# Performance work log

Measured on AMD Instinct MI355X. Metric: run time of the kernel, lower is better.

## Reference

```python
import jax, jax.numpy as jnp
import numpy as np

T, X_D, M_N, CHUNK, REDUCE = 2048, 2048, 64, 64, 8
M_D = X_D // REDUCE          # 256
DECAY_D = M_D // 4           # 64
H_D = X_D * 2                # factor=2
FF_D = 256 * round(int(H_D * (2.0 / 3.0)) / 256)  # 2816


def setup_inputs() -> dict:
    key = jax.random.key(0)
    ks = jax.random.split(key, 20)
    def lin(k, out_d, in_d):
        return (jax.random.normal(k, (out_d, in_d), jnp.float32) / np.sqrt(in_d).astype(np.float32))
    return {
        "xs": jax.random.normal(ks[0], (T, X_D), jnp.float32),
        "attn_q": lin(ks[1], X_D // REDUCE, X_D),
        "attn_k": lin(ks[2], X_D // REDUCE, X_D // REDUCE),
        "attn_v": lin(ks[3], X_D, X_D),
        "attn_o": lin(ks[4], X_D, X_D),
        "attn_r": lin(ks[5], X_D, X_D),
        "mem_f": lin(ks[6], M_N, X_D),
        "mem_q": lin(ks[7], M_D, X_D),
        "mem_k": lin(ks[8], M_D, M_D),
        "mem_v": lin(ks[9], M_D, X_D),
        "mem_o": lin(ks[10], X_D, M_D),
        "mem_r": lin(ks[11], X_D, X_D),
        "mem_beta": -jnp.ones((M_N, M_D), jnp.float32),
        "mem_decay": 3.0 * jnp.ones((M_N, DECAY_D), jnp.float32),
        "mem_l": jax.random.uniform(ks[12], (M_N, M_D), dtype=jnp.float32),
        "ff_in1": lin(ks[13], FF_D, X_D),
        "ff_in2": lin(ks[14], FF_D, X_D),
        "ff_out": lin(ks[15], X_D, FF_D),
        "sn1_g": jnp.sqrt(jnp.float32(X_D)),
        "sn2_g": jnp.sqrt(jnp.float32(X_D)),
    }


def _rotate_half(x):
    x1 = x[..., ::2]
    x2 = x[..., 1::2]
    return jnp.stack((-x2, x1), axis=-1).reshape(x.shape)


def _scale_norm(x, g):
    return x * (g / (jnp.linalg.norm(x, axis=-1, keepdims=True) + 1e-8))


def _attn(xs, Wq, Wk, Wv, Wo, Wr):
    n = CHUNK
    q = xs @ Wq.T                       # (T, dk)
    k = q @ Wk.T                        # k is computed from q (as in source)
    v = xs @ Wv.T                       # (T, x_d)
    c = xs.shape[0] // n
    dk = q.shape[-1]
    q = q.reshape(c, n, dk)
    k = k.reshape(c, n, dk)
    v = v.reshape(c, n, v.shape[-1])

    def with_prev(a):                   # prepend previous chunk (zero for chunk 0)
        prev = jnp.concatenate([jnp.zeros_like(a[:1]), a[:-1]], axis=0)
        return jnp.concatenate([prev, a], axis=1)   # (c, 2n, d)

    k2, v2 = with_prev(k), with_prev(v)

    # RoPE over 2n key positions; queries take the last n positions
    inv_freq = 1.0 / (10000.0 ** (jnp.arange(0, dk, 2, dtype=jnp.float32) / dk))
    ang = jnp.arange(2 * n, dtype=jnp.float32)[:, None] * inv_freq[None, :]
    sin = jnp.repeat(jnp.sin(ang), 2, axis=-1)      # (2n, dk) interleaved
    cos = jnp.repeat(jnp.cos(ang), 2, axis=-1)
    q = q * cos[None, n:] + _rotate_half(q) * sin[None, n:]
    k2 = k2 * cos[None] + _rotate_half(k2) * sin[None]

    qk = jnp.einsum('cnk,cmk->cnm', q, k2) / jnp.sqrt(jnp.float32(dk))
    allowed = jnp.arange(2 * n)[None, :] <= (jnp.arange(n)[:, None] + n)  # tril offset n
    A = jax.nn.softmax(jnp.where(allowed[None], qk, -jnp.inf), axis=-1)
    y = jnp.einsum('cnm,cmv->cnv', A, v2).reshape(xs.shape[0], -1)
    return (y @ Wo.T) * jax.nn.sigmoid(xs @ Wr.T)


def _mem(xs, Wf, Wq, Wk, Wv, Wo, Wr, beta_p, decay_p, l_p):
    v = xs @ Wv.T                                       # (T, m_d)
    f = jax.nn.sigmoid(xs @ Wf.T)[:, :, None]           # (T, m_n, 1)
    beta = jax.nn.sigmoid(beta_p)[None]                 # (1, m_n, m_d)
    gamma = jnp.concatenate(
        [jnp.ones((M_N, M_D - DECAY_D), xs.dtype), jax.nn.sigmoid(decay_p)], axis=1
    )[None]                                             # (1, m_n, m_d)
    ws = (1.0 - f * beta) * gamma                       # (T, m_n, m_d)
    fvs = f * v[:, None, :]                             # (T, m_n, m_d)

    def bin_assoc(ei, ej):
        ai, bi = ei
        aj, bj = ej
        return (aj * ai, aj * bi + bj)

    _, mems = jax.lax.associative_scan(bin_assoc, (ws, fvs), axis=0)  # (T, m_n, m_d)

    q = xs @ Wq.T                                       # (T, m_d)
    k = jnp.einsum('nmd,kd->nmk', mems, Wk) + l_p[None]
    A = jax.nn.softmax(jnp.einsum('nmk,nk->nm', k, q) / jnp.sqrt(jnp.float32(M_D)), axis=-1)
    y = jnp.einsum('nm,nmd->nd', A, mems)
    return (y @ Wo.T) * jax.nn.sigmoid(xs @ Wr.T)


def _ff(xs, W1, W2, Wo):
    return (jax.nn.silu(xs @ W1.T) * (xs @ W2.T)) @ Wo.T


def reference(xs, attn_q, attn_k, attn_v, attn_o, attn_r,
              mem_f, mem_q, mem_k, mem_v, mem_o, mem_r,
              mem_beta, mem_decay, mem_l,
              ff_in1, ff_in2, ff_out, sn1_g, sn2_g):
    xn = _scale_norm(xs, sn1_g)
    xs = (_attn(xn, attn_q, attn_k, attn_v, attn_o, attn_r)
          + _mem(xn, mem_f, mem_q, mem_k, mem_v, mem_o, mem_r, mem_beta, mem_decay, mem_l)
          + xs)
    xs = _ff(_scale_norm(xs, sn2_g), ff_in1, ff_in2, ff_out) + xs
    return xs
```

## Files before the change

kernel.cpp:

```cpp
#include <hip/hip_runtime.h>
#include <math.h>


typedef short bhalf8 __attribute__((ext_vector_type(8)));
typedef float f32x4 __attribute__((ext_vector_type(4)));

#define CC_LD 7168
#define COL_V   0
#define COL_B1  2048
#define COL_B2  4096
#define COL_QB  6144
#define COL_VM  6400
#define COL_QM  6656
#define COL_FG  6912

#define AS1 __attribute__((address_space(1)))
#define AS3 __attribute__((address_space(3)))

__device__ __forceinline__ float sigmoidf_(float x){ return 1.0f/(1.0f+expf(-x)); }

__device__ __forceinline__ unsigned short f2b(float f){
  unsigned u = __float_as_uint(f);
  unsigned r = (u + 0x7fffu + ((u>>16)&1u)) >> 16;
  return (unsigned short)r;
}
__device__ __forceinline__ float b2f(unsigned short h){
  return __uint_as_float(((unsigned)h)<<16);
}

__global__ __launch_bounds__(256) void k_prep(
    const float* __restrict__ av, const float* __restrict__ ar, const float* __restrict__ mr,
    const float* __restrict__ aq, const float* __restrict__ mv, const float* __restrict__ mq,
    const float* __restrict__ mf, const float* __restrict__ ao, const float* __restrict__ mo,
    const float* __restrict__ f1, const float* __restrict__ f2, const float* __restrict__ fo,
    const float* __restrict__ ak, const float* __restrict__ mk,
    const float* __restrict__ xsrc, const float* __restrict__ g1,
    unsigned short* __restrict__ WCAT, unsigned short* __restrict__ AOB,
    unsigned short* __restrict__ MOB, unsigned short* __restrict__ FFW,
    unsigned short* __restrict__ FFOB, unsigned short* __restrict__ AKB,
    unsigned short* __restrict__ MKTB, float2* __restrict__ TR,
    unsigned short* __restrict__ XNb){
  int bid = blockIdx.x, tid = threadIdx.x;
  if (bid < 35520){
    int i = bid*256 + tid;
    const float* s; unsigned short* d; int off;
    if (i < 3571712){
      d = WCAT + (size_t)i*4;
      if      (i < 1048576){ s = av; off = i; }
      else if (i < 2097152){ s = ar; off = i-1048576; }
      else if (i < 3145728){ s = mr; off = i-2097152; }
      else if (i < 3276800){ s = aq; off = i-3145728; }
      else if (i < 3407872){ s = mv; off = i-3276800; }
      else if (i < 3538944){ s = mq; off = i-3407872; }
      else                 { s = mf; off = i-3538944; }
    }
    else if (i < 4620288){ off = i-3571712; s = ao; d = AOB  + (size_t)off*4; }
    else if (i < 4751360){ off = i-4620288; s = mo; d = MOB  + (size_t)off*4; }
    else if (i < 6193152){ off = i-4751360; s = f1;
      int row = off >> 9, c4 = off & 511;
      d = FFW + ((size_t)row*2)*2048 + c4*4; }
    else if (i < 7634944){ off = i-6193152; s = f2;
      int row = off >> 9, c4 = off & 511;
      d = FFW + ((size_t)row*2 + 1)*2048 + c4*4; }
    else if (i < 9076736){ off = i-7634944; s = fo; d = FFOB + (size_t)off*4; }
    else if (i < 9093120){ off = i-9076736; s = ak; d = AKB  + (size_t)off*4; }
    else return;
    float4 v = ((const float4*)s)[off];
    ushort4 o;
    o.x = f2b(v.x); o.y = f2b(v.y); o.z = f2b(v.z); o.w = f2b(v.w);
    *(ushort4*)d = o;
  } else if (bid < 35776){
    int i = bid - 35520, j = tid;
    MKTB[(size_t)j*256 + i] = f2b(mk[(size_t)i*256 + j]);
  } else if (bid < 35840){
    int idx = (bid - 35776)*256 + tid;
    int pos = idx >> 7, j = idx & 127;
    float inv = powf(10000.f, -(float)j/128.f);
    float a = (float)pos * inv;
    TR[idx] = make_float2(cosf(a), sinf(a));
  } else {
    int row = bid - 35840;
    const float* xr = xsrc + (size_t)row*2048;
    float ss = 0.f;
    for (int j = tid; j < 2048; j += 256){ float v = xr[j]; ss += v*v; }
    __shared__ float red[256];
    red[tid] = ss; __syncthreads();
    for (int s = 128; s > 0; s >>= 1){ if (tid < s) red[tid] += red[tid+s]; __syncthreads(); }
    float scale = g1[0] / (sqrtf(red[0]) + 1e-8f);
    unsigned short* orow = XNb + (size_t)row*2048;
    for (int j4 = tid; j4 < 512; j4 += 256){
      float4 v = *(const float4*)(xr + j4*4);
      ushort4 o;
      o.x = f2b(v.x*scale); o.y = f2b(v.y*scale); o.z = f2b(v.z*scale); o.w = f2b(v.w*scale);
      ((ushort4*)orow)[j4] = o;
    }
  }
}

__global__ __launch_bounds__(256) void k_scalenorm_b(const float* __restrict__ x,
    const float* __restrict__ g, unsigned short* __restrict__ ob){
  int row = blockIdx.x, tid = threadIdx.x;
  const float* xr = x + (size_t)row*2048;
  float ss = 0.f;
  for (int j = tid; j < 2048; j += 256){ float v = xr[j]; ss += v*v; }
  __shared__ float red[256];
  red[tid] = ss; __syncthreads();
  for (int s = 128; s > 0; s >>= 1){ if (tid < s) red[tid] += red[tid+s]; __syncthreads(); }
  float scale = g[0] / (sqrtf(red[0]) + 1e-8f);
  unsigned short* orow = ob + (size_t)row*2048;
  for (int j4 = tid; j4 < 512; j4 += 256){
    float4 v = *(const float4*)(xr + j4*4);
    ushort4 o;
    o.x = f2b(v.x*scale); o.y = f2b(v.y*scale); o.z = f2b(v.z*scale); o.w = f2b(v.w*scale);
    ((ushort4*)orow)[j4] = o;
  }
}

__global__ __launch_bounds__(256) void k_gemm_p(
    const unsigned short* __restrict__ A, int lda,
    const unsigned short* __restrict__ B,
    float* __restrict__ C, unsigned short* __restrict__ Cb,
    int N, int K, int ldc, int epi,
    const float* __restrict__ add,
    const unsigned short* __restrict__ gate, int gate_ld,
    const unsigned short* A2, const unsigned short* B2, float* C2){
  __shared__ unsigned short LDSu[24576];
  int tid = threadIdx.x;
  int w = tid >> 6, l = tid & 63;
  int bi = blockIdx.y, bj = blockIdx.x;
  const unsigned short* Ap = A; const unsigned short* Bp = B; float* Cp = C;
  if (blockIdx.z){ Ap = A2; Bp = B2; Cp = C2; }
  int m0 = bi*128, n0 = bj*128;
  int wr = w >> 1, wc = w & 1;

  f32x4 acc[4][4];
#pragma unroll
  for (int i=0;i<4;++i)
#pragma unroll
    for (int j=0;j<4;++j){ f32x4 z = {0.f,0.f,0.f,0.f}; acc[i][j] = z; }

  const int r0 = tid >> 2;
  const int gsrc8 = (((tid&3) ^ ((tid>>3)&3)) * 8);

  auto stage = [&](int bs, int kt){
    unsigned short* db = LDSu + bs*8192;
    const unsigned short* ap0 = Ap + (size_t)(m0 + r0)*lda      + kt*32 + gsrc8;
    const unsigned short* ap1 = Ap + (size_t)(m0 + 64 + r0)*lda + kt*32 + gsrc8;
    const unsigned short* bp0 = Bp + (size_t)(n0 + r0)*K        + kt*32 + gsrc8;
    const unsigned short* bp1 = Bp + (size_t)(n0 + 64 + r0)*K   + kt*32 + gsrc8;
    __builtin_amdgcn_global_load_lds((const AS1 void*)ap0, (AS3 void*)(db + tid*8),        16, 0, 0);
    __builtin_amdgcn_global_load_lds((const AS1 void*)ap1, (AS3 void*)(db + 2048 + tid*8), 16, 0, 0);
    __builtin_amdgcn_global_load_lds((const AS1 void*)bp0, (AS3 void*)(db + 4096 + tid*8), 16, 0, 0);
    __builtin_amdgcn_global_load_lds((const AS1 void*)bp1, (AS3 void*)(db + 6144 + tid*8), 16, 0, 0);
  };

  const int nt = K >> 5;
  stage(0, 0);
  stage(1, 1);
  asm volatile("s_waitcnt vmcnt(4)" ::: "memory");
  __builtin_amdgcn_s_barrier();

  const int lr = l & 15;
  const int gsw = (((l>>4) ^ ((l>>1)&3)) * 8);
  const int aoff = (wr*64 + lr)*32 + gsw;
  const int boff = 4096 + (wc*64 + lr)*32 + gsw;

  int cur = 0;
  for (int t = 0; t < nt; ++t){
    if (t + 2 < nt) stage((t+2)%3, t+2);
    const unsigned short* Tb = LDSu + cur*8192;
    bhalf8 af[4], bfr[4];
#pragma unroll
    for (int m=0;m<4;++m) af[m]  = *(const bhalf8*)(Tb + aoff + m*512);
#pragma unroll
    for (int n=0;n<4;++n) bfr[n] = *(const bhalf8*)(Tb + boff + n*512);
    __builtin_amdgcn_s_setprio(1);
#pragma unroll
    for (int m=0;m<4;++m)
#pragma unroll
      for (int n=0;n<4;++n)
        acc[m][n] = __builtin_amdgcn_mfma_f32_16x16x32_bf16(af[m], bfr[n], acc[m][n], 0, 0, 0);
    __builtin_amdgcn_s_setprio(0);
    if (t + 1 < nt){
      if (t + 2 < nt){ asm volatile("s_waitcnt vmcnt(4)" ::: "memory"); }
      else           { asm volatile("s_waitcnt vmcnt(0)" ::: "memory"); }
      __builtin_amdgcn_s_barrier();
      cur = (cur == 2) ? 0 : cur + 1;
    }
  }

#pragma unroll
  for (int m=0;m<4;++m){
    int rowb = m0 + wr*64 + m*16 + ((l>>4)<<2);
#pragma unroll
    for (int r=0;r<4;++r){
      int row = rowb + r;
      size_t rbase = (size_t)row*ldc;
      size_t gbase = (size_t)row*gate_ld;
#pragma unroll
      for (int n=0;n<4;++n){
        int col = n0 + wc*64 + n*16 + (l&15);
        float v = acc[m][n][r];
        if (add) v += add[rbase + col];
        if (epi == 2) v *= sigmoidf_(b2f(gate[gbase + col]));
        if (epi == 3) Cb[rbase + col] = f2b(v);
        else          Cp[rbase + col] = v;
      }
    }
  }
}

__global__ __launch_bounds__(256) void k_combo1(
    const unsigned short* __restrict__ CCb_, const unsigned short* __restrict__ AKB,
    const unsigned short* __restrict__ MKTB, float* __restrict__ K0f, float* __restrict__ QHf,
    const float* __restrict__ beta_p, const float* __restrict__ decay_p,
    float* __restrict__ CP, float* __restrict__ CQ){
  int bid = blockIdx.x, tid = threadIdx.x;
  if (bid < 64){
    __shared__ unsigned short LDSu[24576];
    int w = tid >> 6, l = tid & 63;
    int zz = bid >> 5, bi = (bid >> 1) & 15, bj = bid & 1;
    const unsigned short* Ap = zz ? (CCb_ + COL_QM) : (CCb_ + COL_QB);
    const unsigned short* Bp = zz ? MKTB : AKB;
    float* Cp = zz ? QHf : K0f;
    const int lda = CC_LD, K = 256, ldc = 256;
    int m0 = bi*128, n0 = bj*128;
    int wr = w >> 1, wc = w & 1;

    f32x4 acc[4][4];
#pragma unroll
    for (int i=0;i<4;++i)
#pragma unroll
      for (int j=0;j<4;++j){ f32x4 z = {0.f,0.f,0.f,0.f}; acc[i][j] = z; }

    const int r0 = tid >> 2;
    const int gsrc8 = (((tid&3) ^ ((tid>>3)&3)) * 8);

    auto stage = [&](int bs, int kt){
      unsigned short* db = LDSu + bs*8192;
      const unsigned short* ap0 = Ap + (size_t)(m0 + r0)*lda      + kt*32 + gsrc8;
      const unsigned short* ap1 = Ap + (size_t)(m0 + 64 + r0)*lda + kt*32 + gsrc8;
      const unsigned short* bp0 = Bp + (size_t)(n0 + r0)*K        + kt*32 + gsrc8;
      const unsigned short* bp1 = Bp + (size_t)(n0 + 64 + r0)*K   + kt*32 + gsrc8;
      __builtin_amdgcn_global_load_lds((const AS1 void*)ap0, (AS3 void*)(db + tid*8),        16, 0, 0);
      __builtin_amdgcn_global_load_lds((const AS1 void*)ap1, (AS3 void*)(db + 2048 + tid*8), 16, 0, 0);
      __builtin_amdgcn_global_load_lds((const AS1 void*)bp0, (AS3 void*)(db + 4096 + tid*8), 16, 0, 0);
      __builtin_amdgcn_global_load_lds((const AS1 void*)bp1, (AS3 void*)(db + 6144 + tid*8), 16, 0, 0);
    };

    const int nt = 8;
    stage(0, 0);
    stage(1, 1);
    asm volatile("s_waitcnt vmcnt(4)" ::: "memory");
    __builtin_amdgcn_s_barrier();

    const int lr = l & 15;
    const int gsw = (((l>>4) ^ ((l>>1)&3)) * 8);
    const int aoff = (wr*64 + lr)*32 + gsw;
    const int boff = 4096 + (wc*64 + lr)*32 + gsw;

    int cur = 0;
    for (int t = 0; t < nt; ++t){
      if (t + 2 < nt) stage((t+2)%3, t+2);
      const unsigned short* Tb = LDSu + cur*8192;
      bhalf8 af[4], bfr[4];
#pragma unroll
      for (int m=0;m<4;++m) af[m]  = *(const bhalf8*)(Tb + aoff + m*512);
#pragma unroll
      for (int n=0;n<4;++n) bfr[n] = *(const bhalf8*)(Tb + boff + n*512);
      __builtin_amdgcn_s_setprio(1);
#pragma unroll
      for (int m=0;m<4;++m)
#pragma unroll
        for (int n=0;n<4;++n)
          acc[m][n] = __builtin_amdgcn_mfma_f32_16x16x32_bf16(af[m], bfr[n], acc[m][n], 0, 0, 0);
      __builtin_amdgcn_s_setprio(0);
      if (t + 1 < nt){
        if (t + 2 < nt){ asm volatile("s_waitcnt vmcnt(4)" ::: "memory"); }
        else           { asm volatile("s_waitcnt vmcnt(0)" ::: "memory"); }
        __builtin_amdgcn_s_barrier();
        cur = (cur == 2) ? 0 : cur + 1;
      }
    }

#pragma unroll
    for (int m=0;m<4;++m){
      int rowb = m0 + wr*64 + m*16 + ((l>>4)<<2);
#pragma unroll
      for (int r=0;r<4;++r){
        size_t rbase = (size_t)(rowb + r)*ldc;
#pragma unroll
        for (int n=0;n<4;++n){
          int col = n0 + wc*64 + n*16 + (l&15);
          Cp[rbase + col] = acc[m][n][r];
        }
      }
    }
  } else {
    int idx = bid - 64;
    int c = idx >> 3, mg = idx & 7, d = tid;
    __shared__ float Fs[128];
    if (tid < 128){
      int s = tid >> 3, j = tid & 7;
      Fs[tid] = sigmoidf_(b2f(CCb_[(size_t)(c*16+s)*CC_LD + COL_FG + mg*8 + j]));
    }
    __syncthreads();
    float beta[8], gamma[8], Pa[8], Qa[8];
#pragma unroll
    for (int j=0;j<8;++j){
      int m = mg*8+j;
      beta[j]  = sigmoidf_(beta_p[m*256+d]);
      gamma[j] = (d < 192) ? 1.f : sigmoidf_(decay_p[m*64 + (d-192)]);
      Pa[j] = 1.f; Qa[j] = 0.f;
    }
    for (int s = 0; s < 16; ++s){
      float vm = b2f(CCb_[(size_t)(c*16+s)*CC_LD + COL_VM + d]);
#pragma unroll
      for (int j=0;j<8;++j){
        float f = Fs[s*8+j];
        float w = (1.f - f*beta[j])*gamma[j];
        Pa[j] *= w;
        Qa[j] = w*Qa[j] + f*vm;
      }
    }
#pragma unroll
    for (int j=0;j<8;++j){
      size_t oidx = ((size_t)c*64 + mg*8 + j)*256 + d;
      CP[oidx] = Pa[j]; CQ[oidx] = Qa[j];
    }
  }
}

__global__ __launch_bounds__(256) void k_combo2(
    const unsigned short* __restrict__ CCqb, const float* __restrict__ K0,
    const float2* __restrict__ TR, unsigned short* __restrict__ P,
    const float* __restrict__ CP, const float* __restrict__ CQ, float* __restrict__ SIN){
  int bid = blockIdx.x, tid = threadIdx.x;
  if (bid < 32){
    __shared__ unsigned short Ks[128*256];
    int c = bid;
    for (int it = 0; it < 16; ++it){
      int id = tid + it*256;
      int m = id >> 5;
      int cs = (id & 31) * 8;
      float v[8];
      if (c == 0 && m < 64){
#pragma unroll
        for (int u=0;u<8;++u) v[u] = 0.f;
      } else {
        int gr = (c-1)*64 + m;
        const float* kr = K0 + (size_t)gr*256 + cs;
        float4 x0 = *(const float4*)kr, x1 = *(const float4*)(kr+4);
        v[0]=x0.x; v[1]=x0.y; v[2]=x0.z; v[3]=x0.w;
        v[4]=x1.x; v[5]=x1.y; v[6]=x1.z; v[7]=x1.w;
#pragma unroll
        for (int p2=0;p2<4;++p2){
          float2 t = TR[m*128 + (cs>>1) + p2];
          float e = v[2*p2], o = v[2*p2+1];
          v[2*p2]   = e*t.x - o*t.y;
          v[2*p2+1] = o*t.x + e*t.y;
        }
      }
      unsigned short pk[8];
#pragma unroll
      for (int u=0;u<8;++u) pk[u] = f2b(v[u]);
      int byte = m*512 + ((cs*2) ^ ((m&7)<<4));
      *(bhalf8*)((char*)&Ks[0] + byte) = *(const bhalf8*)pk;
    }
    __syncthreads();

    int w = tid >> 6, l = tid & 63;
    int lr = l & 15, lkg = l >> 4;
    f32x4 acc[8];
#pragma unroll
    for (int n=0;n<8;++n){ f32x4 z = {0.f,0.f,0.f,0.f}; acc[n] = z; }

    int iq = w*16 + lr;
    const unsigned short* qbase = CCqb + (size_t)(c*64 + iq)*CC_LD;
    int pos = 64 + iq;

    for (int kt = 0; kt < 8; ++kt){
      int k0c = kt*32 + lkg*8;
      bhalf8 q8 = *(const bhalf8*)(qbase + k0c);
      float v[8];
#pragma unroll
      for (int u=0;u<8;++u) v[u] = b2f((unsigned short)(((short*)&q8)[u]));
#pragma unroll
      for (int p2=0;p2<4;++p2){
        float2 t = TR[pos*128 + (k0c>>1) + p2];
        float e = v[2*p2], o = v[2*p2+1];
        v[2*p2]   = e*t.x - o*t.y;
        v[2*p2+1] = o*t.x + e*t.y;
      }
      unsigned short pk[8];
#pragma unroll
      for (int u=0;u<8;++u) pk[u] = f2b(v[u]);
      bhalf8 af = *(const bhalf8*)pk;
#pragma unroll
      for (int n=0;n<8;++n){
        int m = n*16 + lr;
        int byte = m*512 + ((k0c*2) ^ ((m&7)<<4));
        bhalf8 bf = *(const bhalf8*)((const char*)&Ks[0] + byte);
        acc[n] = __builtin_amdgcn_mfma_f32_16x16x32_bf16(af, bf, acc[n], 0, 0, 0);
      }
    }

    int i0 = w*16 + lkg*4;
    float mx[4] = {-1e30f,-1e30f,-1e30f,-1e30f};
    float sm[4] = {0.f,0.f,0.f,0.f};
#pragma unroll
    for (int n=0;n<8;++n){
      int col = n*16 + lr;
#pragma unroll
      for (int r=0;r<4;++r){
        float vv = acc[n][r] * (1.f/16.f);
        if (col > i0 + r + 64) vv = -1e30f;
        acc[n][r] = vv;
        mx[r] = fmaxf(mx[r], vv);
      }
    }
#pragma unroll
    for (int s=1; s<16; s<<=1)
#pragma unroll
      for (int r=0;r<4;++r) mx[r] = fmaxf(mx[r], __shfl_xor(mx[r], s));
#pragma unroll
    for (int n=0;n<8;++n)
#pragma unroll
      for (int r=0;r<4;++r){
        float e = expf(acc[n][r] - mx[r]);
        acc[n][r] = e; sm[r] += e;
      }
#pragma unroll
    for (int s=1; s<16; s<<=1)
#pragma unroll
      for (int r=0;r<4;++r) sm[r] += __shfl_xor(sm[r], s);
    float rcp[4];
#pragma unroll
    for (int r=0;r<4;++r) rcp[r] = 1.f/sm[r];

    unsigned short* Pr = P + (size_t)c*8192;
#pragma unroll
    for (int n=0;n<8;++n){
      int col = n*16 + lr;
#pragma unroll
      for (int r=0;r<4;++r)
        Pr[(i0+r)*128 + col] = f2b(acc[n][r]*rcp[r]);
    }
  } else {
    int m = bid - 32, d = tid;
    float S = 0.f;
    for (int c = 0; c < 128; ++c){
      size_t idx = ((size_t)c*64 + m)*256 + d;
      SIN[idx] = S;
      S = CP[idx]*S + CQ[idx];
    }
  }
}

__global__ __launch_bounds__(256) void k_combo3(
    const unsigned short* __restrict__ P, const unsigned short* __restrict__ Vb, int vld,
    unsigned short* __restrict__ Y,
    const unsigned short* __restrict__ CC, const float* __restrict__ beta_p,
    const float* __restrict__ decay_p, const float* __restrict__ SIN,
    unsigned short* __restrict__ MEMS){
  int bid = blockIdx.x, tid = threadIdx.x;
  if (bid < 512){
    __shared__ unsigned short Vt[128*128];
    int ct = bid & 15, c = bid >> 4;
    {
      int k = tid >> 1;
      int ch = (tid & 1) * 64;
      if (c == 0 && k < 64){
        for (int u=0; u<64; ++u){
          int col = ch + u;
          int byte = col*256 + ((k*2) ^ ((col&7)<<4));
          *(unsigned short*)((char*)&Vt[0] + byte) = 0;
        }
      } else {
        int gr = (c-1)*64 + k;
        const unsigned short* vr = Vb + (size_t)gr*vld + ct*128 + ch;
        for (int u8=0; u8<8; ++u8){
          bhalf8 x = *(const bhalf8*)(vr + u8*8);
#pragma unroll
          for (int u=0;u<8;++u){
            int col = ch + u8*8 + u;
            int byte = col*256 + ((k*2) ^ ((col&7)<<4));
            *(unsigned short*)((char*)&Vt[0] + byte) = (unsigned short)(((short*)&x)[u]);
          }
        }
      }
    }
    __syncthreads();
    int w = tid >> 6, l = tid & 63, lr = l & 15, lkg = l >> 4;
    f32x4 acc[8];
#pragma unroll
    for (int n=0;n<8;++n){ f32x4 z = {0.f,0.f,0.f,0.f}; acc[n] = z; }
    const unsigned short* Pr = P + (size_t)c*8192;
    for (int kt=0; kt<4; ++kt){
      int kb = kt*32 + lkg*8;
      bhalf8 af = *(const bhalf8*)(Pr + (w*16 + lr)*128 + kb);
#pragma unroll
      for (int n=0;n<8;++n){
        int col = n*16 + lr;
        int byte = col*256 + ((kb*2) ^ ((col&7)<<4));
        bhalf8 bf = *(const bhalf8*)((const char*)&Vt[0] + byte);
        acc[n] = __builtin_amdgcn_mfma_f32_16x16x32_bf16(af, bf, acc[n], 0, 0, 0);
      }
    }
    int row0 = c*64 + w*16 + lkg*4;
#pragma unroll
    for (int n=0;n<8;++n){
      int col = ct*128 + n*16 + lr;
#pragma unroll
      for (int r=0;r<4;++r)
        Y[(size_t)(row0+r)*2048 + col] = f2b(acc[n][r]);
    }
  } else {
    int idx = bid - 512;
    int c = idx >> 3, mg = idx & 7, d = tid;
    __shared__ float Fs[128];
    if (tid < 128){
      int s = tid >> 3, j = tid & 7;
      Fs[tid] = sigmoidf_(b2f(CC[(size_t)(c*16+s)*CC_LD + COL_FG + mg*8 + j]));
    }
    __syncthreads();
    float beta[8], gamma[8], S[8];
#pragma unroll
    for (int j=0;j<8;++j){
      int m = mg*8+j;
      beta[j]  = sigmoidf_(beta_p[m*256+d]);
      gamma[j] = (d < 192) ? 1.f : sigmoidf_(decay_p[m*64 + (d-192)]);
      S[j] = SIN[((size_t)c*64 + m)*256 + d];
    }
    for (int s = 0; s < 16; ++s){
      float vm = b2f(CC[(size_t)(c*16+s)*CC_LD + COL_VM + d]);
      size_t tb = (size_t)(c*16+s)*64;
#pragma unroll
      for (int j=0;j<8;++j){
        float f = Fs[s*8+j];
        float w = (1.f - f*beta[j])*gamma[j];
        S[j] = w*S[j] + f*vm;
        MEMS[(tb + mg*8 + j)*256 + d] = f2b(S[j]);
      }
    }
  }
}

__global__ __launch_bounds__(256) void k_gemm_p64(
    const unsigned short* __restrict__ A, int lda,
    const unsigned short* __restrict__ B,
    float* __restrict__ C, int K, int ldc,
    const float* __restrict__ add){
  __shared__ unsigned short LDSu[18432];
  int tid = threadIdx.x;
  int w = tid >> 6, l = tid & 63;
  int bi = blockIdx.y, bj = blockIdx.x;
  int m0 = bi*128, n0 = bj*64;
  int wr = w >> 1, wc = w & 1;

  f32x4 acc[4][2];
#pragma unroll
  for (int i=0;i<4;++i)
#pragma unroll
    for (int j=0;j<2;++j){ f32x4 z = {0.f,0.f,0.f,0.f}; acc[i][j] = z; }

  const int r0 = tid >> 2;
  const int gsrc8 = (((tid&3) ^ ((tid>>3)&3)) * 8);

  auto stage = [&](int bs, int kt){
    unsigned short* db = LDSu + bs*6144;
    const unsigned short* ap0 = A + (size_t)(m0 + r0)*lda      + kt*32 + gsrc8;
    const unsigned short* ap1 = A + (size_t)(m0 + 64 + r0)*lda + kt*32 + gsrc8;
    const unsigned short* bp0 = B + (size_t)(n0 + r0)*K        + kt*32 + gsrc8;
    __builtin_amdgcn_global_load_lds((const AS1 void*)ap0, (AS3 void*)(db + tid*8),        16, 0, 0);
    __builtin_amdgcn_global_load_lds((const AS1 void*)ap1, (AS3 void*)(db + 2048 + tid*8), 16, 0, 0);
    __builtin_amdgcn_global_load_lds((const AS1 void*)bp0, (AS3 void*)(db + 4096 + tid*8), 16, 0, 0);
  };

  const int nt = K >> 5;
  stage(0, 0);
  stage(1, 1);
  asm volatile("s_waitcnt vmcnt(3)" ::: "memory");
  __builtin_amdgcn_s_barrier();

  const int lr = l & 15;
  const int gsw = (((l>>4) ^ ((l>>1)&3)) * 8);
  const int aoff = (wr*64 + lr)*32 + gsw;
  const int boff = 4096 + (wc*32 + lr)*32 + gsw;

  int cur = 0;
  for (int t = 0; t < nt; ++t){
    if (t + 2 < nt) stage((t+2)%3, t+2);
    const unsigned short* Tb = LDSu + cur*6144;
    bhalf8 af[4], bfr[2];
#pragma unroll
    for (int m=0;m<4;++m) af[m]  = *(const bhalf8*)(Tb + aoff + m*512);
#pragma unroll
    for (int n=0;n<2;++n) bfr[n] = *(const bhalf8*)(Tb + boff + n*512);
    __builtin_amdgcn_s_setprio(1);
#pragma unroll
    for (int m=0;m<4;++m)
#pragma unroll
      for (int n=0;n<2;++n)
        acc[m][n] = __builtin_amdgcn_mfma_f32_16x16x32_bf16(af[m], bfr[n], acc[m][n], 0, 0, 0);
    __builtin_amdgcn_s_setprio(0);
    if (t + 1 < nt){
      if (t + 2 < nt){ asm volatile("s_waitcnt vmcnt(3)" ::: "memory"); }
      else           { asm volatile("s_waitcnt vmcnt(0)" ::: "memory"); }
      __builtin_amdgcn_s_barrier();
      cur = (cur == 2) ? 0 : cur + 1;
    }
  }

#pragma unroll
  for (int m=0;m<4;++m){
    int rowb = m0 + wr*64 + m*16 + ((l>>4)<<2);
#pragma unroll
    for (int r=0;r<4;++r){
      int row = rowb + r;
      size_t rbase = (size_t)row*ldc;
#pragma unroll
      for (int n=0;n<2;++n){
        int col = n0 + wc*32 + n*16 + (l&15);
        C[rbase + col] = acc[m][n][r] + add[rbase + col];
      }
    }
  }
}

__global__ __launch_bounds__(256) void k_gemm_fuse2_64(
    const unsigned short* __restrict__ A,  const unsigned short* __restrict__ B,
    const unsigned short* __restrict__ A2, const unsigned short* __restrict__ B2,
    const unsigned short* __restrict__ gate1, const unsigned short* __restrict__ gate2,
    const float* __restrict__ xs, float* __restrict__ XS2){
  __shared__ unsigned short LDSu[18432];
  int tid = threadIdx.x;
  int w = tid >> 6, l = tid & 63;
  int bi = blockIdx.y, bj = blockIdx.x;
  int m0 = bi*128, n0 = bj*64;
  int wr = w >> 1, wc = w & 1;

  f32x4 acc[4][2], acc2[4][2];
#pragma unroll
  for (int i=0;i<4;++i)
#pragma unroll
    for (int j=0;j<2;++j){ f32x4 z = {0.f,0.f,0.f,0.f}; acc[i][j] = z; acc2[i][j] = z; }

  const int r0 = tid >> 2;
  const int gsrc8 = (((tid&3) ^ ((tid>>3)&3)) * 8);

  auto stage = [&](int bs, int kt, const unsigned short* Ap, int lda,
                   const unsigned short* Bp, int ldb){
    unsigned short* db = LDSu + bs*6144;
    const unsigned short* ap0 = Ap + (size_t)(m0 + r0)*lda      + kt*32 + gsrc8;
    const unsigned short* ap1 = Ap + (size_t)(m0 + 64 + r0)*lda + kt*32 + gsrc8;
    const unsigned short* bp0 = Bp + (size_t)(n0 + r0)*ldb      + kt*32 + gsrc8;
    __builtin_amdgcn_global_load_lds((const AS1 void*)ap0, (AS3 void*)(db + tid*8),        16, 0, 0);
    __builtin_amdgcn_global_load_lds((const AS1 void*)ap1, (AS3 void*)(db + 2048 + tid*8), 16, 0, 0);
    __builtin_amdgcn_global_load_lds((const AS1 void*)bp0, (AS3 void*)(db + 4096 + tid*8), 16, 0, 0);
  };

  const int lr = l & 15;
  const int gsw = (((l>>4) ^ ((l>>1)&3)) * 8);
  const int aoff = (wr*64 + lr)*32 + gsw;
  const int boff = 4096 + (wc*32 + lr)*32 + gsw;

  {
    const int nt = 64;
    stage(0, 0, A, 2048, B, 2048);
    stage(1, 1, A, 2048, B, 2048);
    asm volatile("s_waitcnt vmcnt(3)" ::: "memory");
    __builtin_amdgcn_s_barrier();
    int cur = 0;
    for (int t = 0; t < nt; ++t){
      if (t + 2 < nt) stage((t+2)%3, t+2, A, 2048, B, 2048);
      const unsigned short* Tb = LDSu + cur*6144;
      bhalf8 af[4], bfr[2];
#pragma unroll
      for (int m=0;m<4;++m) af[m]  = *(const bhalf8*)(Tb + aoff + m*512);
#pragma unroll
      for (int n=0;n<2;++n) bfr[n] = *(const bhalf8*)(Tb + boff + n*512);
      __builtin_amdgcn_s_setprio(1);
#pragma unroll
      for (int m=0;m<4;++m)
#pragma unroll
        for (int n=0;n<2;++n)
          acc[m][n] = __builtin_amdgcn_mfma_f32_16x16x32_bf16(af[m], bfr[n], acc[m][n], 0, 0, 0);
      __builtin_amdgcn_s_setprio(0);
      if (t + 1 < nt){
        if (t + 2 < nt){ asm volatile("s_waitcnt vmcnt(3)" ::: "memory"); }
        else           { asm volatile("s_waitcnt vmcnt(0)" ::: "memory"); }
        __builtin_amdgcn_s_barrier();
        cur = (cur == 2) ? 0 : cur + 1;
      }
    }
  }
  __syncthreads();

  {
    const int nt = 8;
    stage(0, 0, A2, 256, B2, 256);
    stage(1, 1, A2, 256, B2, 256);
    asm volatile("s_waitcnt vmcnt(3)" ::: "memory");
    __builtin_amdgcn_s_barrier();
    int cur = 0;
    for (int t = 0; t < nt; ++t){
      if (t + 2 < nt) stage((t+2)%3, t+2, A2, 256, B2, 256);
      const unsigned short* Tb = LDSu + cur*6144;
      bhalf8 af[4], bfr[2];
#pragma unroll
      for (int m=0;m<4;++m) af[m]  = *(const bhalf8*)(Tb + aoff + m*512);
#pragma unroll
      for (int n=0;n<2;++n) bfr[n] = *(const bhalf8*)(Tb + boff + n*512);
      __builtin_amdgcn_s_setprio(1);
#pragma unroll
      for (int m=0;m<4;++m)
#pragma unroll
        for (int n=0;n<2;++n)
          acc2[m][n] = __builtin_amdgcn_mfma_f32_16x16x32_bf16(af[m], bfr[n], acc2[m][n], 0, 0, 0);
      __builtin_amdgcn_s_setprio(0);
      if (t + 1 < nt){
        if (t + 2 < nt){ asm volatile("s_waitcnt vmcnt(3)" ::: "memory"); }
        else           { asm volatile("s_waitcnt vmcnt(0)" ::: "memory"); }
        __builtin_amdgcn_s_barrier();
        cur = (cur == 2) ? 0 : cur + 1;
      }
    }
  }

#pragma unroll
  for (int m=0;m<4;++m){
    int rowb = m0 + wr*64 + m*16 + ((l>>4)<<2);
#pragma unroll
    for (int r=0;r<4;++r){
      int row = rowb + r;
      size_t gb = (size_t)row*CC_LD;
      size_t rb = (size_t)row*2048;
#pragma unroll
      for (int n=0;n<2;++n){
        int col = n0 + wc*32 + n*16 + (l&15);
        float v = acc[m][n][r]*sigmoidf_(b2f(gate1[gb + col]))
                + acc2[m][n][r]*sigmoidf_(b2f(gate2[gb + col]))
                + xs[rb + col];
        XS2[rb + col] = v;
      }
    }
  }
}

__global__ __launch_bounds__(256) void k_gemm_silu(
    const unsigned short* __restrict__ A, int lda,
    const unsigned short* __restrict__ B,
    unsigned short* __restrict__ Cb, int K, int out_ld){
  __shared__ unsigned short LDSu[24576];
  int tid = threadIdx.x;
  int w = tid >> 6, l = tid & 63;
  int bi = blockIdx.y, bj = blockIdx.x;
  int m0 = bi*128, n0 = bj*128;
  int wr = w >> 1, wc = w & 1;

  f32x4 acc[4][4];
#pragma unroll
  for (int i=0;i<4;++i)
#pragma unroll
    for (int j=0;j<4;++j){ f32x4 z = {0.f,0.f,0.f,0.f}; acc[i][j] = z; }

  const int r0 = tid >> 2;
  const int gsrc8 = (((tid&3) ^ ((tid>>3)&3)) * 8);

  auto stage = [&](int bs, int kt){
    unsigned short* db = LDSu + bs*8192;
    const unsigned short* ap0 = A + (size_t)(m0 + r0)*lda      + kt*32 + gsrc8;
    const unsigned short* ap1 = A + (size_t)(m0 + 64 + r0)*lda + kt*32 + gsrc8;
    const unsigned short* bp0 = B + (size_t)(n0 + r0)*K        + kt*32 + gsrc8;
    const unsigned short* bp1 = B + (size_t)(n0 + 64 + r0)*K   + kt*32 + gsrc8;
    __builtin_amdgcn_global_load_lds((const AS1 void*)ap0, (AS3 void*)(db + tid*8),        16, 0, 0);
    __builtin_amdgcn_global_load_lds((const AS1 void*)ap1, (AS3 void*)(db + 2048 + tid*8), 16, 0, 0);
    __builtin_amdgcn_global_load_lds((const AS1 void*)bp0, (AS3 void*)(db + 4096 + tid*8), 16, 0, 0);
    __builtin_amdgcn_global_load_lds((const AS1 void*)bp1, (AS3 void*)(db + 6144 + tid*8), 16, 0, 0);
  };

  const int nt = K >> 5;
  stage(0, 0);
  stage(1, 1);
  asm volatile("s_waitcnt vmcnt(4)" ::: "memory");
  __builtin_amdgcn_s_barrier();

  const int lr = l & 15;
  const int gsw = (((l>>4) ^ ((l>>1)&3)) * 8);
  const int aoff = (wr*64 + lr)*32 + gsw;
  const int boff = 4096 + (wc*64 + lr)*32 + gsw;

  int cur = 0;
  for (int t = 0; t < nt; ++t){
    if (t + 2 < nt) stage((t+2)%3, t+2);
    const unsigned short* Tb = LDSu + cur*8192;
    bhalf8 af[4], bfr[4];
#pragma unroll
    for (int m=0;m<4;++m) af[m]  = *(const bhalf8*)(Tb + aoff + m*512);
#pragma unroll
    for (int n=0;n<4;++n) bfr[n] = *(const bhalf8*)(Tb + boff + n*512);
    __builtin_amdgcn_s_setprio(1);
#pragma unroll
    for (int m=0;m<4;++m)
#pragma unroll
      for (int n=0;n<4;++n)
        acc[m][n] = __builtin_amdgcn_mfma_f32_16x16x32_bf16(af[m], bfr[n], acc[m][n], 0, 0, 0);
    __builtin_amdgcn_s_setprio(0);
    if (t + 1 < nt){
      if (t + 2 < nt){ asm volatile("s_waitcnt vmcnt(4)" ::: "memory"); }
      else           { asm volatile("s_waitcnt vmcnt(0)" ::: "memory"); }
      __builtin_amdgcn_s_barrier();
      cur = (cur == 2) ? 0 : cur + 1;
    }
  }

#pragma unroll
  for (int m=0;m<4;++m){
    int rowb = m0 + wr*64 + m*16 + ((l>>4)<<2);
#pragma unroll
    for (int r=0;r<4;++r){
      int row = rowb + r;
      size_t gbase = (size_t)row*out_ld;
#pragma unroll
      for (int n=0;n<4;++n){
        int col = n0 + wc*64 + n*16 + (l&15);
        float v = acc[m][n][r];
        float o = __shfl_xor(v, 1);
        if ((l & 1) == 0)
          Cb[gbase + (col>>1)] = f2b(v*sigmoidf_(v)*o);
      }
    }
  }
}

__global__ __launch_bounds__(256) void k_memread(const unsigned short* __restrict__ MEMS,
    const float* __restrict__ QH, const unsigned short* __restrict__ QMs, int qm_ld,
    const float* __restrict__ L, unsigned short* __restrict__ YMb){
  int t = blockIdx.x, tid = threadIdx.x;
  int wave = tid >> 6, lane = tid & 63;
  __shared__ float anorm[64];
  __shared__ float red2[4][64][4];
  const unsigned short* Mt = MEMS + (size_t)t*16384;
  float4 qh4 = *(const float4*)(QH + (size_t)t*256 + lane*4);
  ushort4 qmu = *(const ushort4*)(QMs + (size_t)t*qm_ld + lane*4);
  float qm0 = b2f(qmu.x), qm1 = b2f(qmu.y), qm2 = b2f(qmu.z), qm3 = b2f(qmu.w);
  for (int mi = 0; mi < 16; ++mi){
    int m = wave*16 + mi;
    ushort4 su = *(const ushort4*)(Mt + m*256 + lane*4);
    float4 l4 = *(const float4*)(L + (size_t)m*256 + lane*4);
    float p = b2f(su.x)*qh4.x + b2f(su.y)*qh4.y + b2f(su.z)*qh4.z + b2f(su.w)*qh4.w
            + l4.x*qm0 + l4.y*qm1 + l4.z*qm2 + l4.w*qm3;
#pragma unroll
    for (int off = 32; off > 0; off >>= 1) p += __shfl_down(p, off);
    if (lane == 0) anorm[m] = p * (1.f/16.f);
  }
  __syncthreads();
  if (tid < 64){
    float v = anorm[tid];
    float mx = v;
#pragma unroll
    for (int off = 32; off > 0; off >>= 1) mx = fmaxf(mx, __shfl_xor(mx, off));
    float e = expf(v - mx);
    float s = e;
#pragma unroll
    for (int off = 32; off > 0; off >>= 1) s += __shfl_xor(s, off);
    anorm[tid] = e / s;
  }
  __syncthreads();
  int mq = tid >> 6, dq = tid & 63;
  float a0=0.f, a1=0.f, a2=0.f, a3=0.f;
#pragma unroll
  for (int mi = 0; mi < 16; ++mi){
    int m = mq*16 + mi;
    ushort4 su = *(const ushort4*)(Mt + m*256 + dq*4);
    float wgt = anorm[m];
    a0 += wgt*b2f(su.x); a1 += wgt*b2f(su.y);
    a2 += wgt*b2f(su.z); a3 += wgt*b2f(su.w);
  }
  red2[mq][dq][0]=a0; red2[mq][dq][1]=a1; red2[mq][dq][2]=a2; red2[mq][dq][3]=a3;
  __syncthreads();
  if (tid < 64){
    float r0=0.f, r1=0.f, r2=0.f, r3=0.f;
#pragma unroll
    for (int g=0; g<4; ++g){
      r0 += red2[g][tid][0]; r1 += red2[g][tid][1];
      r2 += red2[g][tid][2]; r3 += red2[g][tid][3];
    }
    ushort4 o;
    o.x = f2b(r0); o.y = f2b(r1); o.z = f2b(r2); o.w = f2b(r3);
    *(ushort4*)(YMb + (size_t)t*256 + tid*4) = o;
  }
}

extern "C" void kernel_launch(void* const* d_in, const int* in_sizes, int n_in,
                              void* d_out, int out_size, void* d_ws, size_t ws_size,
                              hipStream_t stream){
  const float* xs        = (const float*)d_in[0];
  const float* attn_q    = (const float*)d_in[1];
  const float* attn_k    = (const float*)d_in[2];
  const float* attn_v    = (const float*)d_in[3];
  const float* attn_o    = (const float*)d_in[4];
  const float* attn_r    = (const float*)d_in[5];
  const float* mem_f     = (const float*)d_in[6];
  const float* mem_q     = (const float*)d_in[7];
  const float* mem_k     = (const float*)d_in[8];
  const float* mem_v     = (const float*)d_in[9];
  const float* mem_o     = (const float*)d_in[10];
  const float* mem_r     = (const float*)d_in[11];
  const float* mem_beta  = (const float*)d_in[12];
  const float* mem_decay = (const float*)d_in[13];
  const float* mem_l     = (const float*)d_in[14];
  const float* ff1       = (const float*)d_in[15];
  const float* ff2       = (const float*)d_in[16];
  const float* ffo       = (const float*)d_in[17];
  const float* sn1       = (const float*)d_in[18];
  const float* sn2       = (const float*)d_in[19];
  float* out = (float*)d_out;
  float* W = (float*)d_ws;

  unsigned short* XNb  = (unsigned short*)(W + 0);
  unsigned short* WCAT = (unsigned short*)(W + 2097152);
  unsigned short* CCb  = (unsigned short*)(W + 9437184);
  unsigned short* AOB  = (unsigned short*)(W + 16777216);
  unsigned short* MOB  = (unsigned short*)(W + 18874368);
  unsigned short* FFW  = (unsigned short*)(W + 19136512);
  unsigned short* FFOB = (unsigned short*)(W + 24903680);
  unsigned short* AKB  = (unsigned short*)(W + 27787264);
  unsigned short* MKTB = (unsigned short*)(W + 27820032);
  unsigned short* Ybb  = (unsigned short*)(W + 27852800);
  float*          XS2  = W + 34144256;
  unsigned short* MEMSb= (unsigned short*)(W + 38338560);
  float*          CP   = W + 55115776;
  float*          CQ   = W + 57212928;
  float*          SIN  = W + 59310080;
  float2*         TRIG = (float2*)(W + 61407232);
  float*          K0   = W + 32768;
  unsigned short* P    = (unsigned short*)(W + 557056);
  float*          QH   = W + 688128;
  unsigned short* YMb  = (unsigned short*)(W + 1212416);
  unsigned short* XN2b = MEMSb;
  unsigned short* H1b  = (unsigned short*)(W + 40435712);

  dim3 blk(256);

  k_prep<<<dim3(37888), blk, 0, stream>>>(attn_v, attn_r, mem_r, attn_q, mem_v, mem_q,
      mem_f, attn_o, mem_o, ff1, ff2, ffo, attn_k, mem_k, xs, sn1,
      WCAT, AOB, MOB, FFW, FFOB, AKB, MKTB, TRIG, XNb);

  k_gemm_p<<<dim3(56, 16), blk, 0, stream>>>(XNb, 2048, WCAT, nullptr, CCb, CC_LD, 2048, CC_LD, 3,
      nullptr, nullptr, 0, nullptr, nullptr, nullptr);

  k_combo1<<<dim3(1088), blk, 0, stream>>>(CCb, AKB, MKTB, K0, QH,
      mem_beta, mem_decay, CP, CQ);

  k_combo2<<<dim3(96), blk, 0, stream>>>(CCb + COL_QB, K0, TRIG, P, CP, CQ, SIN);

  k_combo3<<<dim3(1536), blk, 0, stream>>>(P, CCb + COL_V, CC_LD, Ybb,
      CCb, mem_beta, mem_decay, SIN, MEMSb);

  k_memread<<<dim3(2048), blk, 0, stream>>>(MEMSb, QH, CCb + COL_QM, CC_LD, mem_l, YMb);

  k_gemm_fuse2_64<<<dim3(32, 16), blk, 0, stream>>>(Ybb, AOB, YMb, MOB,
      CCb + COL_B1, CCb + COL_B2, xs, XS2);

  k_scalenorm_b<<<dim3(2048), blk, 0, stream>>>(XS2, sn2, XN2b);

  k_gemm_silu<<<dim3(44, 16), blk, 0, stream>>>(XN2b, 2048, FFW, H1b, 2048, 2816);
  k_gemm_p64<<<dim3(32, 16), blk, 0, stream>>>(H1b, 2816, FFOB, out, 2816, 2048, XS2);
}
```

Measured before the change: 375.0 us.

## Overlap downstream weight bf16 conversion with the first concatenated GEMM

The fp32-to-bf16 conversion of the output-projection and feed-forward weights moves out of the prep kernel into extra blocks of a new combined GEMM kernel. Those blocks run grid-stride conversion loops while the 896 GEMM tiles compute, so memory-bound conversion overlaps compute-bound matrix work. The prep kernel shrinks to converting only the weights the first GEMM needs. The risk is that the conversion blocks compete with the GEMM tiles for bandwidth and CU slots, and that block scheduling order decides how much overlap actually happens.

```diff
diff --git a/kernel.cpp b/kernel.cpp
--- a/kernel.cpp
+++ b/kernel.cpp
@@ -31,55 +31,43 @@
 __global__ __launch_bounds__(256) void k_prep(
     const float* __restrict__ av, const float* __restrict__ ar, const float* __restrict__ mr,
     const float* __restrict__ aq, const float* __restrict__ mv, const float* __restrict__ mq,
-    const float* __restrict__ mf, const float* __restrict__ ao, const float* __restrict__ mo,
-    const float* __restrict__ f1, const float* __restrict__ f2, const float* __restrict__ fo,
-    const float* __restrict__ ak, const float* __restrict__ mk,
+    const float* __restrict__ mf, const float* __restrict__ ak, const float* __restrict__ mk,
     const float* __restrict__ xsrc, const float* __restrict__ g1,
-    unsigned short* __restrict__ WCAT, unsigned short* __restrict__ AOB,
-    unsigned short* __restrict__ MOB, unsigned short* __restrict__ FFW,
-    unsigned short* __restrict__ FFOB, unsigned short* __restrict__ AKB,
+    unsigned short* __restrict__ WCAT, unsigned short* __restrict__ AKB,
     unsigned short* __restrict__ MKTB, float2* __restrict__ TR,
     unsigned short* __restrict__ XNb){
   int bid = blockIdx.x, tid = threadIdx.x;
-  if (bid < 35520){
+  if (bid < 13952){
     int i = bid*256 + tid;
-    const float* s; unsigned short* d; int off;
-    if (i < 3571712){
-      d = WCAT + (size_t)i*4;
-      if      (i < 1048576){ s = av; off = i; }
-      else if (i < 2097152){ s = ar; off = i-1048576; }
-      else if (i < 3145728){ s = mr; off = i-2097152; }
-      else if (i < 3276800){ s = aq; off = i-3145728; }
-      else if (i < 3407872){ s = mv; off = i-3276800; }
-      else if (i < 3538944){ s = mq; off = i-3407872; }
-      else                 { s = mf; off = i-3538944; }
-    }
-    else if (i < 4620288){ off = i-3571712; s = ao; d = AOB  + (size_t)off*4; }
-    else if (i < 4751360){ off = i-4620288; s = mo; d = MOB  + (size_t)off*4; }
-    else if (i < 6193152){ off = i-4751360; s = f1;
-      int row = off >> 9, c4 = off & 511;
-      d = FFW + ((size_t)row*2)*2048 + c4*4; }
-    else if (i < 7634944){ off = i-6193152; s = f2;
-      int row = off >> 9, c4 = off & 511;
-      d = FFW + ((size_t)row*2 + 1)*2048 + c4*4; }
-    else if (i < 9076736){ off = i-7634944; s = fo; d = FFOB + (size_t)off*4; }
-    else if (i < 9093120){ off = i-9076736; s = ak; d = AKB  + (size_t)off*4; }
-    else return;
+    const float* s; int off;
+    if      (i < 1048576){ s = av; off = i; }
+    else if (i < 2097152){ s = ar; off = i-1048576; }
+    else if (i < 3145728){ s = mr; off = i-2097152; }
+    else if (i < 3276800){ s = aq; off = i-3145728; }
+    else if (i < 3407872){ s = mv; off = i-3276800; }
+    else if (i < 3538944){ s = mq; off = i-3407872; }
+    else                 { s = mf; off = i-3538944; }
     float4 v = ((const float4*)s)[off];
     ushort4 o;
     o.x = f2b(v.x); o.y = f2b(v.y); o.z = f2b(v.z); o.w = f2b(v.w);
-    *(ushort4*)d = o;
-  } else if (bid < 35776){
-    int i = bid - 35520, j = tid;
+    *(ushort4*)(WCAT + (size_t)i*4) = o;
+  } else if (bid < 14016){
+    int i = (bid - 13952)*256 + tid;
+    float4 v = ((const float4*)ak)[i];
+    ushort4 o;
+    o.x = f2b(v.x); o.y = f2b(v.y); o.z = f2b(v.z); o.w = f2b(v.w);
+    *(ushort4*)(AKB + (size_t)i*4) = o;
+  } else if (bid < 14272){
+    int i = bid - 14016, j = tid;
     MKTB[(size_t)j*256 + i] = f2b(mk[(size_t)i*256 + j]);
-  } else if (bid < 35840){
-    int idx = (bid - 35776)*256 + tid;
+  } else if (bid < 14336){
+    int idx = (bid - 14272)*256 + tid;
     int pos = idx >> 7, j = idx & 127;
     float inv = powf(10000.f, -(float)j/128.f);
     float a = (float)pos * inv;
     TR[idx] = make_float2(cosf(a), sinf(a));
   } else {
-    int row = bid - 35840;
+    int row = bid - 14336;
     const float* xr = xsrc + (size_t)row*2048;
     float ss = 0.f;
     for (int j = tid; j < 2048; j += 256){ float v = xr[j]; ss += v*v; }
@@ -113,6 +101,114 @@
     ushort4 o;
     o.x = f2b(v.x*scale); o.y = f2b(v.y*scale); o.z = f2b(v.z*scale); o.w = f2b(v.w*scale);
     ((ushort4*)orow)[j4] = o;
+  }
+}
+
+__global__ __launch_bounds__(256) void k_gemm_cc(
+    const unsigned short* __restrict__ A, const unsigned short* __restrict__ B,
+    unsigned short* __restrict__ Cb,
+    const float* __restrict__ ao, const float* __restrict__ mo,
+    const float* __restrict__ f1, const float* __restrict__ f2,
+    const float* __restrict__ fo,
+    unsigned short* __restrict__ AOB, unsigned short* __restrict__ MOB,
+    unsigned short* __restrict__ FFW, unsigned short* __restrict__ FFOB){
+  int bid = blockIdx.x, tid = threadIdx.x;
+  if (bid < 896){
+    __shared__ unsigned short LDSu[24576];
+    int w = tid >> 6, l = tid & 63;
+    int bi = bid / 56, bj = bid % 56;
+    const int lda = 2048, K = 2048, ldc = CC_LD;
+    int m0 = bi*128, n0 = bj*128;
+    int wr = w >> 1, wc = w & 1;
+
+    f32x4 acc[4][4];
+#pragma unroll
+    for (int i=0;i<4;++i)
+#pragma unroll
+      for (int j=0;j<4;++j){ f32x4 z = {0.f,0.f,0.f,0.f}; acc[i][j] = z; }
+
+    const int r0 = tid >> 2;
+    const int gsrc8 = (((tid&3) ^ ((tid>>3)&3)) * 8);
+
+    auto stage = [&](int bs, int kt){
+      unsigned short* db = LDSu + bs*8192;
+      const unsigned short* ap0 = A + (size_t)(m0 + r0)*lda      + kt*32 + gsrc8;
+      const unsigned short* ap1 = A + (size_t)(m0 + 64 + r0)*lda + kt*32 + gsrc8;
+      const unsigned short* bp0 = B + (size_t)(n0 + r0)*K        + kt*32 + gsrc8;
+      const unsigned short* bp1 = B + (size_t)(n0 + 64 + r0)*K   + kt*32 + gsrc8;
+      __builtin_amdgcn_global_load_lds((const AS1 void*)ap0, (AS3 void*)(db + tid*8),        16, 0, 0);
+      __builtin_amdgcn_global_load_lds((const AS1 void*)ap1, (AS3 void*)(db + 2048 + tid*8), 16, 0, 0);
+      __builtin_amdgcn_global_load_lds((const AS1 void*)bp0, (AS3 void*)(db + 4096 + tid*8), 16, 0, 0);
+      __builtin_amdgcn_global_load_lds((const AS1 void*)bp1, (AS3 void*)(db + 6144 + tid*8), 16, 0, 0);
+    };
+
+    const int nt = 64;
+    stage(0, 0);
+    stage(1, 1);
+    asm volatile("s_waitcnt vmcnt(4)" ::: "memory");
+    __builtin_amdgcn_s_barrier();
+
+    const int lr = l & 15;
+    const int gsw = (((l>>4) ^ ((l>>1)&3)) * 8);
+    const int aoff = (wr*64 + lr)*32 + gsw;
+    const int boff = 4096 + (wc*64 + lr)*32 + gsw;
+
+    int cur = 0;
+    for (int t = 0; t < nt; ++t){
+      if (t + 2 < nt) stage((t+2)%3, t+2);
+      const unsigned short* Tb = LDSu + cur*8192;
+      bhalf8 af[4], bfr[4];
+#pragma unroll
+      for (int m=0;m<4;++m) af[m]  = *(const bhalf8*)(Tb + aoff + m*512);
+#pragma unroll
+      for (int n=0;n<4;++n) bfr[n] = *(const bhalf8*)(Tb + boff + n*512);
+      __builtin_amdgcn_s_setprio(1);
+#pragma unroll
+      for (int m=0;m<4;++m)
+#pragma unroll
+        for (int n=0;n<4;++n)
+          acc[m][n] = __builtin_amdgcn_mfma_f32_16x16x32_bf16(af[m], bfr[n], acc[m][n], 0, 0, 0);
+      __builtin_amdgcn_s_setprio(0);
+      if (t + 1 < nt){
+        if (t + 2 < nt){ asm volatile("s_waitcnt vmcnt(4)" ::: "memory"); }
+        else           { asm volatile("s_waitcnt vmcnt(0)" ::: "memory"); }
+        __builtin_amdgcn_s_barrier();
+        cur = (cur == 2) ? 0 : cur + 1;
+      }
+    }
+
+#pragma unroll
+    for (int m=0;m<4;++m){
+      int rowb = m0 + wr*64 + m*16 + ((l>>4)<<2);
+#pragma unroll
+      for (int r=0;r<4;++r){
+        size_t rbase = (size_t)(rowb + r)*ldc;
+#pragma unroll
+        for (int n=0;n<4;++n){
+          int col = n0 + wc*64 + n*16 + (l&15);
+          Cb[rbase + col] = f2b(acc[m][n][r]);
+        }
+      }
+    }
+  } else {
+    const int TOT = 5505024;
+    const int stride = 896*256;
+    for (int i = (bid-896)*256 + tid; i < TOT; i += stride){
+      const float* s; unsigned short* d; int off;
+      if (i < 1048576){ s = ao; off = i; d = AOB + (size_t)off*4; }
+      else if (i < 1179648){ s = mo; off = i-1048576; d = MOB + (size_t)off*4; }
+      else if (i < 2621440){ off = i-1179648; s = f1;
+        int row = off >> 9, c4 = off & 511;
+        d = FFW + ((size_t)row*2)*2048 + c4*4; }
+      else if (i < 4063232){ off = i-2621440; s = f2;
+        int row = off >> 9, c4 = off & 511;
+        d = FFW + ((size_t)row*2 + 1)*2048 + c4*4; }
+      else { off = i-4063232; s = fo; d = FFOB + (size_t)off*4; }
+      float4 v = ((const float4*)s)[off];
+      ushort4 o;
+      o.x = f2b(v.x); o.y = f2b(v.y); o.z = f2b(v.z); o.w = f2b(v.w);
+      *(ushort4*)d = o;
+    }
   }
 }
 
@@ -944,12 +1040,11 @@
 
   dim3 blk(256);
 
-  k_prep<<<dim3(37888), blk, 0, stream>>>(attn_v, attn_r, mem_r, attn_q, mem_v, mem_q,
-      mem_f, attn_o, mem_o, ff1, ff2, ffo, attn_k, mem_k, xs, sn1,
-      WCAT, AOB, MOB, FFW, FFOB, AKB, MKTB, TRIG, XNb);
-
-  k_gemm_p<<<dim3(56, 16), blk, 0, stream>>>(XNb, 2048, WCAT, nullptr, CCb, CC_LD, 2048, CC_LD, 3,
-      nullptr, nullptr, 0, nullptr, nullptr, nullptr);
+  k_prep<<<dim3(16384), blk, 0, stream>>>(attn_v, attn_r, mem_r, attn_q, mem_v, mem_q,
+      mem_f, attn_k, mem_k, xs, sn1, WCAT, AKB, MKTB, TRIG, XNb);
+
+  k_gemm_cc<<<dim3(1792), blk, 0, stream>>>(XNb, WCAT, CCb,
+      attn_o, mem_o, ff1, ff2, ffo, AOB, MOB, FFW, FFOB);
 
   k_combo1<<<dim3(1088), blk, 0, stream>>>(CCb, AKB, MKTB, K0, QH,
       mem_beta, mem_decay, CP, CQ);
```

After: 386.3 us. 3.0% more time.
